# Optimization experiments

Hardware: AMD Instinct MI355X
Metric: run time of the kernel (lower is better)

The kernel has to match this reference:

```python
import jax, jax.numpy as jnp
import numpy as np

N_NODES = 100000

def _gcn_conv(x, edge_index, W, b):
    # PyG GCNConv with normalize=False, add_self_loops=False:
    # out[dst] = sum_{(src,dst) in E} (x @ W)[src] + b
    xw = x @ W                                   # [N, out]
    src, dst = edge_index[0], edge_index[1]
    agg = jax.ops.segment_sum(xw[src], dst, num_segments=x.shape[0])  # [N, out]
    return agg + b

def setup_inputs() -> dict:
    key = jax.random.key(0)
    k1, k2, k3, k4 = jax.random.split(key, 4)
    F_in, F_hid, F_out = 128, 64, 40
    E = 1_600_000
    x = jax.random.normal(k1, (N_NODES, F_in), dtype=jnp.float32)
    edge_index = jax.random.randint(k2, (2, E), 0, N_NODES, dtype=jnp.int64)
    W1 = jax.random.normal(k3, (F_in, F_hid), dtype=jnp.float32) * (1.0 / np.sqrt(F_in))
    b1 = jnp.zeros((F_hid,), dtype=jnp.float32)
    W2 = jax.random.normal(k4, (F_hid, F_out), dtype=jnp.float32) * (1.0 / np.sqrt(F_hid))
    b2 = jnp.zeros((F_out,), dtype=jnp.float32)
    return {"x": x, "edge_index": edge_index, "W1": W1, "b1": b1, "W2": W2, "b2": b2}

def reference(x, edge_index, W1, b1, W2, b2):
    h = _gcn_conv(x, edge_index, W1, b1)
    h = jax.nn.relu(h)
    h = _gcn_conv(h, edge_index, W2, b2)
    return jax.nn.log_softmax(h, axis=1)
```

## Files before the change

### kernel.cpp

```cpp
#include <hip/hip_runtime.h>
#include <cstdint>
#include <cstddef>

#define F_IN  128
#define F_HID 64
#define F_OUT 40

#define BSH   9
#define NBMAX 256
#define CHUNK 4096

#define BLD_T   512
#define BLD_CAP 10240

typedef __attribute__((ext_vector_type(8))) short short8;
typedef __attribute__((ext_vector_type(4))) float f32x4;

__device__ __forceinline__ unsigned short f2bf(float f) {
  unsigned u = __float_as_uint(f);
  u += 0x7fffu + ((u >> 16) & 1u);
  return (unsigned short)(u >> 16);
}
__device__ __forceinline__ float bf2f(unsigned short b) {
  return __uint_as_float((unsigned)b << 16);
}
__device__ __forceinline__ float bflo(unsigned u) { return __uint_as_float(u << 16); }
__device__ __forceinline__ float bfhi(unsigned u) { return __uint_as_float(u & 0xffff0000u); }
__device__ __forceinline__ unsigned packbf(float lo, float hi) {
  return (unsigned)f2bf(lo) | ((unsigned)f2bf(hi) << 16);
}

__global__ __launch_bounds__(256) void front_k(const float* __restrict__ x,
                                               const float* __restrict__ W1,
                                               const float* __restrict__ W2,
                                               unsigned short* __restrict__ w2s,
                                               unsigned short* __restrict__ xw, int N,
                                               const int* __restrict__ ei,
                                               int* __restrict__ counts,
                                               int E, int NBLK, int NBUCK) {
  __shared__ int lh[NBMAX];
  __shared__ unsigned short w1l[8192];
  int t = threadIdx.x;

  if ((int)blockIdx.x < NBLK) {
    int blk = blockIdx.x;
    lh[t] = 0;
    __syncthreads();
    int e0 = blk * CHUNK;
    int n = min(CHUNK, E - e0);
    for (int i = t; i < n; i += 256)
      atomicAdd(&lh[((unsigned)ei[E + e0 + i]) >> BSH], 1);
    __syncthreads();
    if (t < NBUCK) counts[t * NBLK + blk] = lh[t];
    if (blk == 0) {
      for (int i = t; i < 3072; i += 256) {
        int f = i >> 9, r = i & 511;
        int lane = r >> 3, j = r & 7;
        int ct = f >> 1, ks = f & 1;
        int n2 = ct * 16 + (lane & 15);
        int k = ks * 32 + (lane >> 4) * 8 + j;
        w2s[i] = (n2 < F_OUT) ? f2bf(W2[k * F_OUT + n2]) : (unsigned short)0;
      }
    }
    return;
  }

  {
    int k = t >> 1, n0 = (t & 1) * 32;
    const float4* wp = (const float4*)(W1 + k * F_HID + n0);
    float4 v[8];
#pragma unroll
    for (int u = 0; u < 8; ++u) v[u] = wp[u];
#pragma unroll
    for (int u = 0; u < 32; ++u) {
      int n = n0 + u;
      float f = ((const float*)v)[u];
      int idx = ((n >> 4) * 4 + (k >> 5)) * 512 +
                (((k >> 3) & 3) * 16 + (n & 15)) * 8 + (k & 7);
      w1l[idx] = f2bf(f);
    }
  }
  __syncthreads();

  int gblk = blockIdx.x - NBLK;
  int lane = t & 63;
  int wid  = gblk * 4 + (t >> 6);
  int row0 = wid * 16;
  if (row0 >= N) return;
  int m = lane & 15, q = lane >> 4;

  if (row0 + 16 <= N) {
    short8 b[16];
#pragma unroll
    for (int f = 0; f < 16; ++f)
      b[f] = *(const short8*)(w1l + f * 512 + lane * 8);

    short8 a[4];
#pragma unroll
    for (int ks = 0; ks < 4; ++ks) {
      const float* xp = x + (size_t)(row0 + m) * F_IN + ks * 32 + q * 8;
      float4 v0 = *(const float4*)xp;
      float4 v1 = *(const float4*)(xp + 4);
      short8 tt;
      tt[0] = (short)f2bf(v0.x); tt[1] = (short)f2bf(v0.y);
      tt[2] = (short)f2bf(v0.z); tt[3] = (short)f2bf(v0.w);
      tt[4] = (short)f2bf(v1.x); tt[5] = (short)f2bf(v1.y);
      tt[6] = (short)f2bf(v1.z); tt[7] = (short)f2bf(v1.w);
      a[ks] = tt;
    }

    f32x4 z = {0.f, 0.f, 0.f, 0.f};
    f32x4 acc[4] = {z, z, z, z};
#pragma unroll
    for (int ct = 0; ct < 4; ++ct)
#pragma unroll
      for (int ks = 0; ks < 4; ++ks)
        acc[ct] = __builtin_amdgcn_mfma_f32_16x16x32_bf16(a[ks], b[ct * 4 + ks],
                                                          acc[ct], 0, 0, 0);
#pragma unroll
    for (int ct = 0; ct < 4; ++ct)
#pragma unroll
      for (int r = 0; r < 4; ++r) {
        int row = row0 + q * 4 + r;
        xw[(size_t)row * F_HID + ct * 16 + m] = f2bf(acc[ct][r]);
      }
  } else {
    for (int r = 0; r < 16 && row0 + r < N; ++r) {
      const float* xr = x + (size_t)(row0 + r) * F_IN;
      float s = 0.f;
      for (int k = 0; k < F_IN; ++k) s = fmaf(xr[k], W1[k * F_HID + lane], s);
      xw[(size_t)(row0 + r) * F_HID + lane] = f2bf(s);
    }
  }
}

__global__ __launch_bounds__(256) void scanA_k(const int* __restrict__ a,
                                               int* __restrict__ psum, int M) {
  int t = threadIdx.x;
  int base = blockIdx.x * 2048 + t * 8;
  int s = 0;
#pragma unroll
  for (int j = 0; j < 8; ++j) if (base + j < M) s += a[base + j];
#pragma unroll
  for (int off = 32; off; off >>= 1) s += __shfl_xor(s, off, 64);
  __shared__ int sm[4];
  if ((t & 63) == 0) sm[t >> 6] = s;
  __syncthreads();
  if (t == 0) psum[blockIdx.x] = sm[0] + sm[1] + sm[2] + sm[3];
}

__global__ __launch_bounds__(256) void scanC_k(int* __restrict__ a,
                                               const int* __restrict__ psum,
                                               int M, int E, int nb) {
  __shared__ int sb[256];
  __shared__ int sm[256];
  int t = threadIdx.x;

  int pv = (t < nb) ? psum[t] : 0;
  sb[t] = pv;
  __syncthreads();
  for (int off = 1; off < 256; off <<= 1) {
    int add = (t >= off) ? sb[t - off] : 0;
    __syncthreads();
    sb[t] += add;
    __syncthreads();
  }
  int excl = sb[t] - pv;
  __syncthreads();
  sb[t] = excl;
  __syncthreads();
  int blockBase = sb[blockIdx.x];

  int base = blockIdx.x * 2048 + t * 8;
  int v[8];
  int s = 0;
#pragma unroll
  for (int j = 0; j < 8; ++j) {
    v[j] = (base + j < M) ? a[base + j] : 0;
    s += v[j];
  }
  sm[t] = s;
  __syncthreads();
  for (int off = 1; off < 256; off <<= 1) {
    int add = (t >= off) ? sm[t - off] : 0;
    __syncthreads();
    sm[t] += add;
    __syncthreads();
  }
  int run = blockBase + sm[t] - s;
#pragma unroll
  for (int j = 0; j < 8; ++j) {
    if (base + j < M) a[base + j] = run;
    run += v[j];
  }
  if (blockIdx.x == 0 && t == 0) a[M] = E;
}

__global__ __launch_bounds__(256) void partition_k(const int* __restrict__ bases,
                                                   const int* __restrict__ ei,
                                                   unsigned* __restrict__ ebuf,
                                                   int E, int NBLK, int NBUCK) {
  __shared__ uint2 slots[CHUNK];
  __shared__ int scn[NBMAX], lcur[NBMAX], gadj[NBMAX];
  int t = threadIdx.x, blk = blockIdx.x;
  int e0 = blk * CHUNK;
  int n = min(CHUNK, E - e0);

  int i0 = t * NBLK + blk;
  int cnt = 0, base0 = 0;
  if (t < NBUCK) {
    base0 = bases[i0];
    cnt = bases[i0 + 1] - base0;
  }
  scn[t] = cnt;
  __syncthreads();
  for (int off = 1; off < 256; off <<= 1) {
    int add = (t >= off) ? scn[t - off] : 0;
    __syncthreads();
    scn[t] += add;
    __syncthreads();
  }
  int excl = scn[t] - cnt;
  if (t < NBUCK) { lcur[t] = excl; gadj[t] = base0 - excl; }
  __syncthreads();

  for (int i = t; i < n; i += 256) {
    int s = ei[e0 + i], d = ei[E + e0 + i];
    int pos = atomicAdd(&lcur[((unsigned)d) >> BSH], 1);
    slots[pos] = make_uint2((unsigned)s, (unsigned)d);
  }
  __syncthreads();
  for (int i = t; i < n; i += 256) {
    uint2 sd = slots[i];
    unsigned pk = ((sd.y & 511u) << 17) | sd.x;
    ebuf[gadj[sd.y >> BSH] + i] = pk;
  }
}

__global__ __launch_bounds__(BLD_T) void build_k(const unsigned* __restrict__ ebuf,
                                                 const int* __restrict__ bases,
                                                 int* __restrict__ row_ptr,
                                                 int* __restrict__ csr,
                                                 int N, int E, int NBLK) {
  __shared__ int hist[512];
  __shared__ int psc[256];
  __shared__ unsigned stg[BLD_CAP];
  int t = threadIdx.x, b = blockIdx.x;
  int nodeBase = b << BSH;
  int S = bases[b * NBLK];
  int T = bases[(b + 1) * NBLK];
  int n = T - S;
  bool useLds = (n <= BLD_CAP);

  if (t < 512) hist[t] = 0;
  __syncthreads();
  for (int i = t; i < n; i += BLD_T) {
    unsigned v = ebuf[S + i];
    if (useLds) stg[i] = v;
    atomicAdd(&hist[v >> 17], 1);
  }
  __syncthreads();

  int v0 = 0, v1 = 0, pair = 0;
  if (t < 256) {
    v0 = hist[2 * t]; v1 = hist[2 * t + 1];
    pair = v0 + v1;
    psc[t] = pair;
  }
  __syncthreads();
  for (int off = 1; off < 256; off <<= 1) {
    int add = (t >= off && t < 256) ? psc[t - off] : 0;
    __syncthreads();
    if (t < 256) psc[t] += add;
    __syncthreads();
  }
  if (t < 256) {
    int ep = psc[t] - pair;
    int e0 = ep, e1 = ep + v0;
    int node0 = nodeBase + 2 * t;
    if (node0 < N) row_ptr[node0] = S + e0;
    if (node0 + 1 < N) row_ptr[node0 + 1] = S + e1;
    hist[2 * t] = e0; hist[2 * t + 1] = e1;
  }
  if (b == 0 && t == 0) row_ptr[N] = E;
  __syncthreads();
  for (int i = t; i < n; i += BLD_T) {
    unsigned v = useLds ? stg[i] : ebuf[S + i];
    int pos = atomicAdd(&hist[v >> 17], 1);
    csr[S + pos] = (int)(v & 0x1FFFFu);
  }
}

__global__ __launch_bounds__(256) void agg1g2_k(const unsigned short* __restrict__ xw,
                                                const int* __restrict__ row_ptr,
                                                const int* __restrict__ csr,
                                                const float* __restrict__ b1,
                                                const unsigned short* __restrict__ w2s,
                                                const float* __restrict__ W2,
                                                unsigned short* __restrict__ hw, int N) {
  __shared__ uint4 hsm[32][8];
  int t = threadIdx.x;
  int wave = t >> 6, lane = t & 63;
  int blockRow0 = blockIdx.x * 32;
  int rowBase = blockRow0 + wave * 8;
  int row = rowBase + (lane >> 3);
  int part = lane & 7;
  bool live = row < N;

  int start = live ? row_ptr[row] : 0;
  int end   = live ? row_ptr[row + 1] : 0;

  float acc[8], bcc[8];
#pragma unroll
  for (int j = 0; j < 8; ++j) { acc[j] = 0.f; bcc[j] = 0.f; }

  int i = start;
  for (; i + 3 < end; i += 4) {
    int s0 = csr[i];
    int s1 = csr[i + 1];
    int s2 = csr[i + 2];
    int s3 = csr[i + 3];
    uint4 v0 = *(const uint4*)(xw + ((size_t)s0 << 6) + (part << 3));
    uint4 v1 = *(const uint4*)(xw + ((size_t)s1 << 6) + (part << 3));
    uint4 v2 = *(const uint4*)(xw + ((size_t)s2 << 6) + (part << 3));
    uint4 v3 = *(const uint4*)(xw + ((size_t)s3 << 6) + (part << 3));
    acc[0] += bflo(v0.x); acc[1] += bfhi(v0.x);
    acc[2] += bflo(v0.y); acc[3] += bfhi(v0.y);
    acc[4] += bflo(v0.z); acc[5] += bfhi(v0.z);
    acc[6] += bflo(v0.w); acc[7] += bfhi(v0.w);
    bcc[0] += bflo(v1.x); bcc[1] += bfhi(v1.x);
    bcc[2] += bflo(v1.y); bcc[3] += bfhi(v1.y);
    bcc[4] += bflo(v1.z); bcc[5] += bfhi(v1.z);
    bcc[6] += bflo(v1.w); bcc[7] += bfhi(v1.w);
    acc[0] += bflo(v2.x); acc[1] += bfhi(v2.x);
    acc[2] += bflo(v2.y); acc[3] += bfhi(v2.y);
    acc[4] += bflo(v2.z); acc[5] += bfhi(v2.z);
    acc[6] += bflo(v2.w); acc[7] += bfhi(v2.w);
    bcc[0] += bflo(v3.x); bcc[1] += bfhi(v3.x);
    bcc[2] += bflo(v3.y); bcc[3] += bfhi(v3.y);
    bcc[4] += bflo(v3.z); bcc[5] += bfhi(v3.z);
    bcc[6] += bflo(v3.w); bcc[7] += bfhi(v3.w);
  }
  for (; i < end; ++i) {
    int s = csr[i];
    uint4 v = *(const uint4*)(xw + ((size_t)s << 6) + (part << 3));
    acc[0] += bflo(v.x); acc[1] += bfhi(v.x);
    acc[2] += bflo(v.y); acc[3] += bfhi(v.y);
    acc[4] += bflo(v.z); acc[5] += bfhi(v.z);
    acc[6] += bflo(v.w); acc[7] += bfhi(v.w);
  }

  if (live) {
    int c0 = part << 3;
    float4 bA = *(const float4*)(b1 + c0);
    float4 bB = *(const float4*)(b1 + c0 + 4);
    float r0 = fmaxf(acc[0] + bcc[0] + bA.x, 0.f);
    float r1 = fmaxf(acc[1] + bcc[1] + bA.y, 0.f);
    float r2 = fmaxf(acc[2] + bcc[2] + bA.z, 0.f);
    float r3 = fmaxf(acc[3] + bcc[3] + bA.w, 0.f);
    float r4 = fmaxf(acc[4] + bcc[4] + bB.x, 0.f);
    float r5 = fmaxf(acc[5] + bcc[5] + bB.y, 0.f);
    float r6 = fmaxf(acc[6] + bcc[6] + bB.z, 0.f);
    float r7 = fmaxf(acc[7] + bcc[7] + bB.w, 0.f);
    uint4 o = make_uint4(packbf(r0, r1), packbf(r2, r3), packbf(r4, r5), packbf(r6, r7));
    int lr = row - blockRow0;
    hsm[lr][part ^ (lr & 7)] = o;
  }
  __syncthreads();

  if (wave < 2) {
    int frow0 = blockRow0 + wave * 16;
    if (frow0 >= N) return;
    int m = lane & 15, q = lane >> 4;
    if (frow0 + 16 <= N) {
      short8 b[6];
#pragma unroll
      for (int f = 0; f < 6; ++f)
        b[f] = *(const short8*)(w2s + f * 512 + lane * 8);
      short8 a[2];
#pragma unroll
      for (int ks = 0; ks < 2; ++ks) {
        int lr = wave * 16 + m;
        int p = ks * 4 + q;
        a[ks] = *(const short8*)&hsm[lr][p ^ (lr & 7)];
      }
      f32x4 z = {0.f, 0.f, 0.f, 0.f};
      f32x4 acc2[3] = {z, z, z};
#pragma unroll
      for (int ct = 0; ct < 3; ++ct)
#pragma unroll
        for (int ks = 0; ks < 2; ++ks)
          acc2[ct] = __builtin_amdgcn_mfma_f32_16x16x32_bf16(a[ks], b[ct * 2 + ks],
                                                             acc2[ct], 0, 0, 0);
#pragma unroll
      for (int ct = 0; ct < 3; ++ct)
#pragma unroll
        for (int r = 0; r < 4; ++r) {
          int row2 = frow0 + q * 4 + r;
          int c = ct * 16 + m;
          if (c < F_OUT) hw[(size_t)row2 * F_OUT + c] = f2bf(acc2[ct][r]);
        }
    } else {
      for (int r = 0; r < 16; ++r) {
        int row2 = frow0 + r;
        if (row2 >= N) break;
        if (lane < F_OUT) {
          int lr = wave * 16 + r;
          float s = 0.f;
          for (int k = 0; k < F_HID; ++k) {
            const unsigned short* hp =
                (const unsigned short*)&hsm[lr][(k >> 3) ^ (lr & 7)];
            s = fmaf(bf2f(hp[k & 7]), W2[k * F_OUT + lane], s);
          }
          hw[(size_t)row2 * F_OUT + lane] = f2bf(s);
        }
      }
    }
  }
}

__global__ __launch_bounds__(256) void agg2_ls_k(const unsigned short* __restrict__ hw,
                                                 const int* __restrict__ row_ptr,
                                                 const int* __restrict__ csr,
                                                 const float* __restrict__ b2,
                                                 float* __restrict__ out, int N) {
  int wid = (blockIdx.x * 256 + threadIdx.x) >> 6;
  int lane = threadIdx.x & 63;
  int rowBase = wid * 8;
  if (rowBase >= N) return;
  int row = rowBase + (lane >> 3);
  int part = lane & 7;
  bool live = row < N;
  bool ld = live && (part < 5);

  int start = live ? row_ptr[row] : 0;
  int end   = live ? row_ptr[row + 1] : 0;

  float acc[8], bcc[8];
#pragma unroll
  for (int j = 0; j < 8; ++j) { acc[j] = 0.f; bcc[j] = 0.f; }

  int i = start;
  for (; i + 3 < end; i += 4) {
    int s0 = csr[i];
    int s1 = csr[i + 1];
    int s2 = csr[i + 2];
    int s3 = csr[i + 3];
    if (ld) {
      uint4 v0 = *(const uint4*)(hw + (size_t)s0 * F_OUT + (part << 3));
      uint4 v1 = *(const uint4*)(hw + (size_t)s1 * F_OUT + (part << 3));
      uint4 v2 = *(const uint4*)(hw + (size_t)s2 * F_OUT + (part << 3));
      uint4 v3 = *(const uint4*)(hw + (size_t)s3 * F_OUT + (part << 3));
      acc[0] += bflo(v0.x); acc[1] += bfhi(v0.x);
      acc[2] += bflo(v0.y); acc[3] += bfhi(v0.y);
      acc[4] += bflo(v0.z); acc[5] += bfhi(v0.z);
      acc[6] += bflo(v0.w); acc[7] += bfhi(v0.w);
      bcc[0] += bflo(v1.x); bcc[1] += bfhi(v1.x);
      bcc[2] += bflo(v1.y); bcc[3] += bfhi(v1.y);
      bcc[4] += bflo(v1.z); bcc[5] += bfhi(v1.z);
      bcc[6] += bflo(v1.w); bcc[7] += bfhi(v1.w);
      acc[0] += bflo(v2.x); acc[1] += bfhi(v2.x);
      acc[2] += bflo(v2.y); acc[3] += bfhi(v2.y);
      acc[4] += bflo(v2.z); acc[5] += bfhi(v2.z);
      acc[6] += bflo(v2.w); acc[7] += bfhi(v2.w);
      bcc[0] += bflo(v3.x); bcc[1] += bfhi(v3.x);
      bcc[2] += bflo(v3.y); bcc[3] += bfhi(v3.y);
      bcc[4] += bflo(v3.z); bcc[5] += bfhi(v3.z);
      bcc[6] += bflo(v3.w); bcc[7] += bfhi(v3.w);
    }
  }
  for (; i < end; ++i) {
    int s = csr[i];
    if (ld) {
      uint4 v = *(const uint4*)(hw + (size_t)s * F_OUT + (part << 3));
      acc[0] += bflo(v.x); acc[1] += bfhi(v.x);
      acc[2] += bflo(v.y); acc[3] += bfhi(v.y);
      acc[4] += bflo(v.z); acc[5] += bfhi(v.z);
      acc[6] += bflo(v.w); acc[7] += bfhi(v.w);
    }
  }

  bool valid = ld;
  float vj[8];
  float m = -3.4e38f;
  if (valid) {
    int c0 = part << 3;
    float4 bA = *(const float4*)(b2 + c0);
    float4 bB = *(const float4*)(b2 + c0 + 4);
    vj[0] = acc[0] + bcc[0] + bA.x; vj[1] = acc[1] + bcc[1] + bA.y;
    vj[2] = acc[2] + bcc[2] + bA.z; vj[3] = acc[3] + bcc[3] + bA.w;
    vj[4] = acc[4] + bcc[4] + bB.x; vj[5] = acc[5] + bcc[5] + bB.y;
    vj[6] = acc[6] + bcc[6] + bB.z; vj[7] = acc[7] + bcc[7] + bB.w;
#pragma unroll
    for (int j = 0; j < 8; ++j) m = fmaxf(m, vj[j]);
  }
#pragma unroll
  for (int off = 1; off < 8; off <<= 1) m = fmaxf(m, __shfl_xor(m, off, 64));
  float ex = 0.f;
  if (valid) {
#pragma unroll
    for (int j = 0; j < 8; ++j) ex += __expf(vj[j] - m);
  }
#pragma unroll
  for (int off = 1; off < 8; off <<= 1) ex += __shfl_xor(ex, off, 64);
  float lse = __logf(ex) + m;

  if (valid) {
    int c0 = part << 3;
    float* op = out + (size_t)row * F_OUT + c0;
    *(float4*)op = make_float4(vj[0] - lse, vj[1] - lse, vj[2] - lse, vj[3] - lse);
    *(float4*)(op + 4) = make_float4(vj[4] - lse, vj[5] - lse, vj[6] - lse, vj[7] - lse);
  }
}

extern "C" void kernel_launch(void* const* d_in, const int* in_sizes, int n_in,
                              void* d_out, int out_size, void* d_ws, size_t ws_size,
                              hipStream_t stream) {
  const float* x  = (const float*)d_in[0];
  const int*   ei = (const int*)d_in[1];
  const float* W1 = (const float*)d_in[2];
  const float* b1 = (const float*)d_in[3];
  const float* W2 = (const float*)d_in[4];
  const float* b2 = (const float*)d_in[5];

  int N = in_sizes[0] / F_IN;
  int E = in_sizes[1] / 2;

  char* base = (char*)d_ws;
  size_t szA = (size_t)N * F_HID * sizeof(unsigned short);
  size_t szEb = (size_t)E * sizeof(unsigned);
  size_t szHw = (size_t)N * F_OUT * sizeof(unsigned short);
  size_t szB = (szEb > szHw) ? szEb : szHw;
  unsigned short* xw = (unsigned short*)base;
  char* regB = base + ((szA + 255) & ~(size_t)255);
  unsigned* ebuf       = (unsigned*)regB;
  unsigned short* hw   = (unsigned short*)regB;
  int* row_ptr = (int*)(regB + ((szB + 255) & ~(size_t)255));
  int* csr     = row_ptr + N + 1;
  int* counts  = csr + E;
  float* out = (float*)d_out;

  int aggGrid  = (N * 8 + 255) / 256;
  int gemmGrid = (N + 63) / 64;
  int fusGrid  = (N + 31) / 32;
  int NBLK  = (E + CHUNK - 1) / CHUNK;
  int NBUCK = (N + 511) >> BSH;
  int M = NBUCK * NBLK;
  int* psum = counts + M + 1;
  unsigned short* w2s = (unsigned short*)(psum + 256);
  int scanBlocks = (M + 2047) / 2048;

  front_k<<<NBLK + gemmGrid, 256, 0, stream>>>(x, W1, W2, w2s, xw, N,
                                               ei, counts, E, NBLK, NBUCK);

  scanA_k<<<scanBlocks, 256, 0, stream>>>(counts, psum, M);
  scanC_k<<<scanBlocks, 256, 0, stream>>>(counts, psum, M, E, scanBlocks);
  partition_k<<<NBLK, 256, 0, stream>>>(counts, ei, ebuf, E, NBLK, NBUCK);
  build_k<<<NBUCK, BLD_T, 0, stream>>>(ebuf, counts, row_ptr, csr, N, E, NBLK);

  agg1g2_k<<<fusGrid, 256, 0, stream>>>(xw, row_ptr, csr, b1, w2s, W2, hw, N);
  agg2_ls_k<<<aggGrid, 256, 0, stream>>>(hw, row_ptr, csr, b2, out, N);
}
```

Baseline: 218.4 us.

## Pad layer-2 features to 64 columns, pack 12 rows per wave, single-block scan

The second-layer intermediate hw is now stored with a 64-element row stride, so gather addresses become shifts and every row load is a 16-byte aligned vector. The final aggregation kernel assigns 5 lanes per row and 12 rows per wave instead of 8 lanes with 3 idle, which cuts wasted lanes and grid size. The lanes combine their max and sum for log-softmax with explicit shuffles. The two-kernel counts scan is replaced by a single 1024-thread block scan, which saves a launch but serialises per-thread chunks. The padded layout raises hw storage and write traffic.

```diff
diff --git a/kernel.cpp b/kernel.cpp
--- a/kernel.cpp
+++ b/kernel.cpp
@@ -55,10 +55,10 @@
     if (blk == 0) {
       for (int i = t; i < 3072; i += 256) {
         int f = i >> 9, r = i & 511;
-        int lane = r >> 3, j = r & 7;
+        int lane = r >> 3, jj = r & 7;
         int ct = f >> 1, ks = f & 1;
         int n2 = ct * 16 + (lane & 15);
-        int k = ks * 32 + (lane >> 4) * 8 + j;
+        int k = ks * 32 + (lane >> 4) * 8 + jj;
         w2s[i] = (n2 < F_OUT) ? f2bf(W2[k * F_OUT + n2]) : (unsigned short)0;
       }
     }
@@ -134,66 +134,29 @@
   }
 }
 
-__global__ __launch_bounds__(256) void scanA_k(const int* __restrict__ a,
-                                               int* __restrict__ psum, int M) {
+__global__ __launch_bounds__(1024) void scan1_k(int* __restrict__ a, int M, int E) {
+  __shared__ int sm[1024];
   int t = threadIdx.x;
-  int base = blockIdx.x * 2048 + t * 8;
+  int per = (M + 1023) >> 10;
+  int s0 = t * per;
+  int s1 = min(s0 + per, M);
   int s = 0;
-#pragma unroll
-  for (int j = 0; j < 8; ++j) if (base + j < M) s += a[base + j];
-#pragma unroll
-  for (int off = 32; off; off >>= 1) s += __shfl_xor(s, off, 64);
-  __shared__ int sm[4];
-  if ((t & 63) == 0) sm[t >> 6] = s;
-  __syncthreads();
-  if (t == 0) psum[blockIdx.x] = sm[0] + sm[1] + sm[2] + sm[3];
-}
-
-__global__ __launch_bounds__(256) void scanC_k(int* __restrict__ a,
-                                               const int* __restrict__ psum,
-                                               int M, int E, int nb) {
-  __shared__ int sb[256];
-  __shared__ int sm[256];
-  int t = threadIdx.x;
-
-  int pv = (t < nb) ? psum[t] : 0;
-  sb[t] = pv;
-  __syncthreads();
-  for (int off = 1; off < 256; off <<= 1) {
-    int add = (t >= off) ? sb[t - off] : 0;
-    __syncthreads();
-    sb[t] += add;
-    __syncthreads();
-  }
-  int excl = sb[t] - pv;
-  __syncthreads();
-  sb[t] = excl;
-  __syncthreads();
-  int blockBase = sb[blockIdx.x];
-
-  int base = blockIdx.x * 2048 + t * 8;
-  int v[8];
-  int s = 0;
-#pragma unroll
-  for (int j = 0; j < 8; ++j) {
-    v[j] = (base + j < M) ? a[base + j] : 0;
-    s += v[j];
-  }
+  for (int i = s0; i < s1; ++i) s += a[i];
   sm[t] = s;
   __syncthreads();
-  for (int off = 1; off < 256; off <<= 1) {
+  for (int off = 1; off < 1024; off <<= 1) {
     int add = (t >= off) ? sm[t - off] : 0;
     __syncthreads();
     sm[t] += add;
     __syncthreads();
   }
-  int run = blockBase + sm[t] - s;
-#pragma unroll
-  for (int j = 0; j < 8; ++j) {
-    if (base + j < M) a[base + j] = run;
-    run += v[j];
-  }
-  if (blockIdx.x == 0 && t == 0) a[M] = E;
+  int run = (t > 0) ? sm[t - 1] : 0;
+  for (int i = s0; i < s1; ++i) {
+    int v = a[i];
+    a[i] = run;
+    run += v;
+  }
+  if (t == 0) a[M] = E;
 }
 
 __global__ __launch_bounds__(256) void partition_k(const int* __restrict__ bases,
@@ -362,7 +325,8 @@
     float r5 = fmaxf(acc[5] + bcc[5] + bB.y, 0.f);
     float r6 = fmaxf(acc[6] + bcc[6] + bB.z, 0.f);
     float r7 = fmaxf(acc[7] + bcc[7] + bB.w, 0.f);
-    uint4 o = make_uint4(packbf(r0, r1), packbf(r2, r3), packbf(r4, r5), packbf(r6, r7));
+    uint4 o = make_uint4(packbf(r0, r1), packbf(r2, r3),
+                         packbf(r4, r5), packbf(r6, r7));
     int lr = row - blockRow0;
     hsm[lr][part ^ (lr & 7)] = o;
   }
@@ -381,8 +345,8 @@
 #pragma unroll
       for (int ks = 0; ks < 2; ++ks) {
         int lr = wave * 16 + m;
-        int p = ks * 4 + q;
-        a[ks] = *(const short8*)&hsm[lr][p ^ (lr & 7)];
+        int pp = ks * 4 + q;
+        a[ks] = *(const short8*)&hsm[lr][pp ^ (lr & 7)];
       }
       f32x4 z = {0.f, 0.f, 0.f, 0.f};
       f32x4 acc2[3] = {z, z, z};
@@ -390,15 +354,15 @@
       for (int ct = 0; ct < 3; ++ct)
 #pragma unroll
         for (int ks = 0; ks < 2; ++ks)
-          acc2[ct] = __builtin_amdgcn_mfma_f32_16x16x32_bf16(a[ks], b[ct * 2 + ks],
-                                                             acc2[ct], 0, 0, 0);
+          acc2[ct] = __builtin_amdgcn_mfma_f32_16x16x32_bf16(
+              a[ks], b[ct * 2 + ks], acc2[ct], 0, 0, 0);
 #pragma unroll
       for (int ct = 0; ct < 3; ++ct)
 #pragma unroll
         for (int r = 0; r < 4; ++r) {
           int row2 = frow0 + q * 4 + r;
           int c = ct * 16 + m;
-          if (c < F_OUT) hw[(size_t)row2 * F_OUT + c] = f2bf(acc2[ct][r]);
+          if (c < F_OUT) hw[(size_t)row2 * F_HID + c] = f2bf(acc2[ct][r]);
         }
     } else {
       for (int r = 0; r < 16; ++r) {
@@ -412,7 +376,7 @@
                 (const unsigned short*)&hsm[lr][(k >> 3) ^ (lr & 7)];
             s = fmaf(bf2f(hp[k & 7]), W2[k * F_OUT + lane], s);
           }
-          hw[(size_t)row2 * F_OUT + lane] = f2bf(s);
+          hw[(size_t)row2 * F_HID + lane] = f2bf(s);
         }
       }
     }
@@ -424,14 +388,12 @@
                                                  const int* __restrict__ csr,
                                                  const float* __restrict__ b2,
                                                  float* __restrict__ out, int N) {
-  int wid = (blockIdx.x * 256 + threadIdx.x) >> 6;
-  int lane = threadIdx.x & 63;
-  int rowBase = wid * 8;
-  if (rowBase >= N) return;
-  int row = rowBase + (lane >> 3);
-  int part = lane & 7;
-  bool live = row < N;
-  bool ld = live && (part < 5);
+  int t = threadIdx.x;
+  int wave = t >> 6, lane = t & 63;
+  int grp = lane / 5;
+  int part = lane - grp * 5;
+  int row = blockIdx.x * 48 + wave * 12 + grp;
+  bool live = (grp < 12) && (row < N);
 
   int start = live ? row_ptr[row] : 0;
   int end   = live ? row_ptr[row + 1] : 0;
@@ -446,33 +408,31 @@
     int s1 = csr[i + 1];
     int s2 = csr[i + 2];
     int s3 = csr[i + 3];
-    if (ld) {
-      uint4 v0 = *(const uint4*)(hw + (size_t)s0 * F_OUT + (part << 3));
-      uint4 v1 = *(const uint4*)(hw + (size_t)s1 * F_OUT + (part << 3));
-      uint4 v2 = *(const uint4*)(hw + (size_t)s2 * F_OUT + (part << 3));
-      uint4 v3 = *(const uint4*)(hw + (size_t)s3 * F_OUT + (part << 3));
-      acc[0] += bflo(v0.x); acc[1] += bfhi(v0.x);
-      acc[2] += bflo(v0.y); acc[3] += bfhi(v0.y);
-      acc[4] += bflo(v0.z); acc[5] += bfhi(v0.z);
-      acc[6] += bflo(v0.w); acc[7] += bfhi(v0.w);
-      bcc[0] += bflo(v1.x); bcc[1] += bfhi(v1.x);
-      bcc[2] += bflo(v1.y); bcc[3] += bfhi(v1.y);
-      bcc[4] += bflo(v1.z); bcc[5] += bfhi(v1.z);
-      bcc[6] += bflo(v1.w); bcc[7] += bfhi(v1.w);
-      acc[0] += bflo(v2.x); acc[1] += bfhi(v2.x);
-      acc[2] += bflo(v2.y); acc[3] += bfhi(v2.y);
-      acc[4] += bflo(v2.z); acc[5] += bfhi(v2.z);
-      acc[6] += bflo(v2.w); acc[7] += bfhi(v2.w);
-      bcc[0] += bflo(v3.x); bcc[1] += bfhi(v3.x);
-      bcc[2] += bflo(v3.y); bcc[3] += bfhi(v3.y);
-      bcc[4] += bflo(v3.z); bcc[5] += bfhi(v3.z);
-      bcc[6] += bflo(v3.w); bcc[7] += bfhi(v3.w);
-    }
-  }
-  for (; i < end; ++i) {
-    int s = csr[i];
-    if (ld) {
-      uint4 v = *(const uint4*)(hw + (size_t)s * F_OUT + (part << 3));
+    uint4 v0 = *(const uint4*)(hw + ((size_t)s0 << 6) + (part << 3));
+    uint4 v1 = *(const uint4*)(hw + ((size_t)s1 << 6) + (part << 3));
+    uint4 v2 = *(const uint4*)(hw + ((size_t)s2 << 6) + (part << 3));
+    uint4 v3 = *(const uint4*)(hw + ((size_t)s3 << 6) + (part << 3));
+    acc[0] += bflo(v0.x); acc[1] += bfhi(v0.x);
+    acc[2] += bflo(v0.y); acc[3] += bfhi(v0.y);
+    acc[4] += bflo(v0.z); acc[5] += bfhi(v0.z);
+    acc[6] += bflo(v0.w); acc[7] += bfhi(v0.w);
+    bcc[0] += bflo(v1.x); bcc[1] += bfhi(v1.x);
+    bcc[2] += bflo(v1.y); bcc[3] += bfhi(v1.y);
+    bcc[4] += bflo(v1.z); bcc[5] += bfhi(v1.z);
+    bcc[6] += bflo(v1.w); bcc[7] += bfhi(v1.w);
+    acc[0] += bflo(v2.x); acc[1] += bfhi(v2.x);
+    acc[2] += bflo(v2.y); acc[3] += bfhi(v2.y);
+    acc[4] += bflo(v2.z); acc[5] += bfhi(v2.z);
+    acc[6] += bflo(v2.w); acc[7] += bfhi(v2.w);
+    bcc[0] += bflo(v3.x); bcc[1] += bfhi(v3.x);
+    bcc[2] += bflo(v3.y); bcc[3] += bfhi(v3.y);
+    bcc[4] += bflo(v3.z); bcc[5] += bfhi(v3.z);
+    bcc[6] += bflo(v3.w); bcc[7] += bfhi(v3.w);
+  }
+  if (i < end) {
+    for (; i < end; ++i) {
+      int s = csr[i];
+      uint4 v = *(const uint4*)(hw + ((size_t)s << 6) + (part << 3));
       acc[0] += bflo(v.x); acc[1] += bfhi(v.x);
       acc[2] += bflo(v.y); acc[3] += bfhi(v.y);
       acc[4] += bflo(v.z); acc[5] += bfhi(v.z);
@@ -480,10 +440,9 @@
     }
   }
 
-  bool valid = ld;
   float vj[8];
-  float m = -3.4e38f;
-  if (valid) {
+  float mx = -3.4e38f;
+  if (live) {
     int c0 = part << 3;
     float4 bA = *(const float4*)(b2 + c0);
     float4 bB = *(const float4*)(b2 + c0 + 4);
@@ -492,20 +451,23 @@
     vj[4] = acc[4] + bcc[4] + bB.x; vj[5] = acc[5] + bcc[5] + bB.y;
     vj[6] = acc[6] + bcc[6] + bB.z; vj[7] = acc[7] + bcc[7] + bB.w;
 #pragma unroll
-    for (int j = 0; j < 8; ++j) m = fmaxf(m, vj[j]);
-  }
-#pragma unroll
-  for (int off = 1; off < 8; off <<= 1) m = fmaxf(m, __shfl_xor(m, off, 64));
+    for (int q = 0; q < 8; ++q) mx = fmaxf(mx, vj[q]);
+  }
+  int g0 = (grp < 12 ? grp : 0) * 5;
+  float mxAll = mx;
+#pragma unroll
+  for (int q = 0; q < 5; ++q) mxAll = fmaxf(mxAll, __shfl(mx, g0 + q, 64));
   float ex = 0.f;
-  if (valid) {
-#pragma unroll
-    for (int j = 0; j < 8; ++j) ex += __expf(vj[j] - m);
-  }
-#pragma unroll
-  for (int off = 1; off < 8; off <<= 1) ex += __shfl_xor(ex, off, 64);
-  float lse = __logf(ex) + m;
-
-  if (valid) {
+  if (live) {
+#pragma unroll
+    for (int q = 0; q < 8; ++q) ex += __expf(vj[q] - mxAll);
+  }
+  float exAll = 0.f;
+#pragma unroll
+  for (int q = 0; q < 5; ++q) exAll += __shfl(ex, g0 + q, 64);
+  float lse = __logf(exAll) + mxAll;
+
+  if (live) {
     int c0 = part << 3;
     float* op = out + (size_t)row * F_OUT + c0;
     *(float4*)op = make_float4(vj[0] - lse, vj[1] - lse, vj[2] - lse, vj[3] - lse);
@@ -529,7 +491,7 @@
   char* base = (char*)d_ws;
   size_t szA = (size_t)N * F_HID * sizeof(unsigned short);
   size_t szEb = (size_t)E * sizeof(unsigned);
-  size_t szHw = (size_t)N * F_OUT * sizeof(unsigned short);
+  size_t szHw = (size_t)N * F_HID * sizeof(unsigned short);
   size_t szB = (szEb > szHw) ? szEb : szHw;
   unsigned short* xw = (unsigned short*)base;
   char* regB = base + ((szA + 255) & ~(size_t)255);
@@ -540,24 +502,22 @@
   int* counts  = csr + E;
   float* out = (float*)d_out;
 
-  int aggGrid  = (N * 8 + 255) / 256;
-  int gemmGrid = (N + 63) / 64;
-  int fusGrid  = (N + 31) / 32;
   int NBLK  = (E + CHUNK - 1) / CHUNK;
   int NBUCK = (N + 511) >> BSH;
   int M = NBUCK * NBLK;
-  int* psum = counts + M + 1;
-  unsigned short* w2s = (unsigned short*)(psum + 256);
-  int scanBlocks = (M + 2047) / 2048;
+  unsigned short* w2s =
+      (unsigned short*)(((uintptr_t)(counts + M + 1) + 63) & ~(uintptr_t)63);
+  int gemmGrid = (N + 63) / 64;
+  int aggGrid1 = (N + 31) / 32;
+  int aggGrid2 = (N + 47) / 48;
 
   front_k<<<NBLK + gemmGrid, 256, 0, stream>>>(x, W1, W2, w2s, xw, N,
                                                ei, counts, E, NBLK, NBUCK);
 
-  scanA_k<<<scanBlocks, 256, 0, stream>>>(counts, psum, M);
-  scanC_k<<<scanBlocks, 256, 0, stream>>>(counts, psum, M, E, scanBlocks);
+  scan1_k<<<1, 1024, 0, stream>>>(counts, M, E);
   partition_k<<<NBLK, 256, 0, stream>>>(counts, ei, ebuf, E, NBLK, NBUCK);
   build_k<<<NBUCK, BLD_T, 0, stream>>>(ebuf, counts, row_ptr, csr, N, E, NBLK);
 
-  agg1g2_k<<<fusGrid, 256, 0, stream>>>(xw, row_ptr, csr, b1, w2s, W2, hw, N);
-  agg2_ls_k<<<aggGrid, 256, 0, stream>>>(hw, row_ptr, csr, b2, out, N);
-}
+  agg1g2_k<<<aggGrid1, 256, 0, stream>>>(xw, row_ptr, csr, b1, w2s, W2, hw, N);
+  agg2_ls_k<<<aggGrid2, 256, 0, stream>>>(hw, row_ptr, csr, b2, out, N);
+}
```

New measurement: 331.8 us. 52.0% more time.
